# Kernel tuning notes

Hardware: AMD Instinct MI355X
Metric: run time of the kernel (lower is better)

## Reference

```python
import jax, jax.numpy as jnp
import numpy as np

BETA = 0.9


def setup_inputs() -> dict:
    key = jax.random.key(0)
    ks = jax.random.split(key, 9)
    B, T, D, H, C = 512, 2048, 64, 48, 3
    s = lambda k, shape, fan_in: jax.random.normal(k, shape, jnp.float32) / np.sqrt(fan_in)
    return {
        "x": jax.random.normal(ks[0], (B, T, D), jnp.float32),
        "W_enc": s(ks[1], (H, D), D),
        "b_enc": jnp.zeros((H,), jnp.float32),
        "W_mem": s(ks[2], (H, H), H),
        "b_mem": jnp.zeros((H,), jnp.float32),
        "W_dec": s(ks[3], (D, H), H),
        "b_dec": jnp.zeros((D,), jnp.float32),
        "W_cls": s(ks[4], (C, H), H),
        "b_cls": jnp.zeros((C,), jnp.float32),
    }


def _forward(x, W_enc, b_enc, W_mem, b_mem, W_dec, b_dec, W_cls, b_cls):
    B, T, D = x.shape
    H = W_enc.shape[0]
    # Precompute input drive for all steps in one big matmul: [B, T, H]
    u = jnp.einsum("btd,hd->bth", x, W_enc) + b_enc
    u_t = jnp.swapaxes(u, 0, 1)  # [T, B, H]

    def step(mem, u_step):
        cur = u_step + mem @ W_mem.T + b_mem
        mem = BETA * mem + (1.0 - BETA) * cur
        return mem, jax.nn.sigmoid(mem)

    mem0 = jnp.zeros((B, H), x.dtype)
    _, spikes = jax.lax.scan(step, mem0, u_t)  # spikes: [T, B, H]
    z = jnp.swapaxes(spikes, 0, 1)  # [B, T, H]
    recon = jnp.einsum("bth,dh->btd", z, W_dec) + b_dec
    logits = z.mean(axis=1) @ W_cls.T + b_cls
    return recon, logits, z


def reference(x, W_enc, b_enc, W_mem, b_mem, W_dec, b_dec, W_cls, b_cls):
    return _forward(x, W_enc, b_enc, W_mem, b_mem, W_dec, b_dec, W_cls, b_cls)
```

## Files before the change

### kernel.cpp

```cpp
#include <hip/hip_runtime.h>
#include <cstdint>
#include <cstddef>

#define B_ 512
#define T_ 2048
#define D_ 64
#define H_ 48
#define C_ 3
#define LCH 16
#define KCH 128
#define NC  65536
#define CPB 128
#define SMS 162

#define RECON_FLOATS ((size_t)B_ * T_ * D_)
#define LOGIT_FLOATS ((size_t)B_ * C_)
#define Z_OFF        (RECON_FLOATS + LOGIT_FLOATS)
#define A16_OFF  ((size_t)59768832)

__global__ __launch_bounds__(128) void k_enc(
    const float* __restrict__ x, const float* __restrict__ Wenc,
    const float* __restrict__ benc, const float* __restrict__ bmem,
    float* __restrict__ out)
{
    __shared__ float sx[128][68];
    __shared__ float sw[48][68];
    __shared__ float sbe[48];

    const int tid = threadIdx.x;

    {
        const float4* wf4 = reinterpret_cast<const float4*>(Wenc);
        #pragma unroll
        for (int m = 0; m < 6; ++m) {
            const int idx = tid + 128 * m;
            const int c = idx >> 4, d4 = idx & 15;
            *reinterpret_cast<float4*>(&sw[c][d4 * 4]) = wf4[idx];
        }
    }
    if (tid < 48) sbe[tid] = benc[tid] + bmem[tid];

    {
        const float4* xf4 = reinterpret_cast<const float4*>(x) + (size_t)blockIdx.x * 2048;
        #pragma unroll
        for (int m = 0; m < 16; ++m) {
            const int idx = tid + 128 * m;
            const int row = idx >> 4, d4 = idx & 15;
            *reinterpret_cast<float4*>(&sx[row][d4 * 4]) = xf4[idx];
        }
    }
    __syncthreads();

    const int lane = tid & 63;
    const int wv   = tid >> 6;
    const int rg   = lane >> 2;
    const int cg   = lane & 3;
    const int rowb = wv * 64 + rg;
    const int colb = cg * 12;

    float acc[4][12];
    {
        float bia[12];
        #pragma unroll
        for (int m = 0; m < 3; ++m)
            *reinterpret_cast<float4*>(&bia[4 * m]) = *reinterpret_cast<const float4*>(&sbe[colb + 4 * m]);
        #pragma unroll
        for (int k = 0; k < 4; ++k)
            #pragma unroll
            for (int i = 0; i < 12; ++i) acc[k][i] = bia[i];
    }

    #pragma unroll 2
    for (int d4 = 0; d4 < 16; ++d4) {
        float4 xf[4];
        #pragma unroll
        for (int k = 0; k < 4; ++k)
            xf[k] = *reinterpret_cast<const float4*>(&sx[rowb + 16 * k][d4 * 4]);
        #pragma unroll
        for (int i = 0; i < 12; ++i) {
            const float4 wvv = *reinterpret_cast<const float4*>(&sw[colb + i][d4 * 4]);
            #pragma unroll
            for (int k = 0; k < 4; ++k)
                acc[k][i] = fmaf(xf[k].x, wvv.x, fmaf(xf[k].y, wvv.y,
                             fmaf(xf[k].z, wvv.z, fmaf(xf[k].w, wvv.w, acc[k][i]))));
        }
    }

    const size_t row0 = (size_t)blockIdx.x * 128 + rowb;
    #pragma unroll
    for (int k = 0; k < 4; ++k) {
        float* dst = out + (row0 + 16 * k) * 48 + colb;
        #pragma unroll
        for (int m = 0; m < 3; ++m)
            *reinterpret_cast<float4*>(dst + 4 * m) =
                make_float4(acc[k][4 * m], acc[k][4 * m + 1], acc[k][4 * m + 2], acc[k][4 * m + 3]);
    }
}

__global__ __launch_bounds__(576) void k_powA(
    const float* __restrict__ Wmem, float* __restrict__ out)
{
    __shared__ float a0[48 * 49];
    __shared__ float a1[48 * 49];
    const int tid = threadIdx.x;

    for (int idx = tid; idx < 2304; idx += 576) {
        const int i = idx / 48, j = idx - i * 48;
        a0[i * 49 + j] = 0.1f * Wmem[idx] + (i == j ? 0.9f : 0.0f);
    }
    __syncthreads();

    float* src = a0;
    float* dst = a1;
    #pragma unroll 1
    for (int it = 0; it < 4; ++it) {
        float v[4];
        #pragma unroll
        for (int q = 0; q < 4; ++q) {
            const int o = tid + 576 * q;
            const int i = o / 48, j = o - i * 48;
            float acc = 0.f;
            #pragma unroll
            for (int k = 0; k < 48; ++k)
                acc = fmaf(src[i * 49 + k], src[k * 49 + j], acc);
            v[q] = acc;
        }
        #pragma unroll
        for (int q = 0; q < 4; ++q) {
            const int o = tid + 576 * q;
            const int i = o / 48, j = o - i * 48;
            dst[i * 49 + j] = v[q];
        }
        __syncthreads();
        float* t = src; src = dst; dst = t;
    }
    for (int idx = tid; idx < 2304; idx += 576) {
        const int i = idx / 48, j = idx - i * 48;
        out[A16_OFF + idx] = src[i * 49 + j];
    }
}

#define LOAD_UREG(sidx)                                                         \
    {                                                                           \
        const float* pb = u + (c0 + cbase) * 768 + (size_t)(sidx) * 48 + r0;    \
        _Pragma("unroll")                                                       \
        for (int j = 0; j < 8; ++j) {                                           \
            ureg[j][0] = pb[j * 768 + 0];                                       \
            ureg[j][1] = pb[j * 768 + 1];                                       \
            ureg[j][2] = pb[j * 768 + 2];                                       \
        }                                                                       \
    }

#define GEMM_STEP                                                               \
    float acc[3][8];                                                            \
    _Pragma("unroll")                                                           \
    for (int r = 0; r < 3; ++r)                                                 \
        _Pragma("unroll")                                                       \
        for (int j = 0; j < 8; ++j) acc[r][j] = ureg[j][r];                     \
    LOAD_UREG(s + 1 < LCH ? s + 1 : LCH - 1)                                    \
    _Pragma("unroll")                                                           \
    for (int k4 = 0; k4 < 12; ++k4) {                                           \
        float4 av[3];                                                           \
        _Pragma("unroll")                                                       \
        for (int r = 0; r < 3; ++r)                                             \
            av[r] = *reinterpret_cast<const float4*>(&sA[(r0 + r) * 52 + k4 * 4]); \
        float4 mv0[4], mv1[4];                                                  \
        _Pragma("unroll")                                                       \
        for (int kk = 0; kk < 4; ++kk) {                                        \
            mv0[kk] = *reinterpret_cast<const float4*>(&sM[(k4 * 4 + kk) * SMS + pcb]);     \
            mv1[kk] = *reinterpret_cast<const float4*>(&sM[(k4 * 4 + kk) * SMS + pcb + 4]); \
        }                                                                       \
        _Pragma("unroll")                                                       \
        for (int kk = 0; kk < 4; ++kk) {                                        \
            _Pragma("unroll")                                                   \
            for (int r = 0; r < 3; ++r) {                                       \
                const float a = kk == 0 ? av[r].x : kk == 1 ? av[r].y           \
                              : kk == 2 ? av[r].z : av[r].w;                    \
                acc[r][0] = fmaf(a, mv0[kk].x, acc[r][0]);                      \
                acc[r][1] = fmaf(a, mv0[kk].y, acc[r][1]);                      \
                acc[r][2] = fmaf(a, mv0[kk].z, acc[r][2]);                      \
                acc[r][3] = fmaf(a, mv0[kk].w, acc[r][3]);                      \
                acc[r][4] = fmaf(a, mv1[kk].x, acc[r][4]);                      \
                acc[r][5] = fmaf(a, mv1[kk].y, acc[r][5]);                      \
                acc[r][6] = fmaf(a, mv1[kk].z, acc[r][6]);                      \
                acc[r][7] = fmaf(a, mv1[kk].w, acc[r][7]);                      \
            }                                                                   \
        }                                                                       \
    }

#define WRITE_M                                                                 \
    __syncthreads();                                                            \
    _Pragma("unroll")                                                           \
    for (int r = 0; r < 3; ++r) {                                               \
        *reinterpret_cast<float4*>(&sM[(r0 + r) * SMS + pcb]) =                 \
            make_float4(acc[r][0], acc[r][1], acc[r][2], acc[r][3]);            \
        *reinterpret_cast<float4*>(&sM[(r0 + r) * SMS + pcb + 4]) =             \
            make_float4(acc[r][4], acc[r][5], acc[r][6], acc[r][7]);            \
    }                                                                           \
    __syncthreads();

__global__ __launch_bounds__(256) void k_scan(
    const float* __restrict__ Wmem, const float* __restrict__ A16g,
    const float* __restrict__ Wcls, const float* __restrict__ bcls,
    const float* __restrict__ u, float* __restrict__ z, float* __restrict__ logits)
{
    __shared__ float sA[48 * 52];
    __shared__ float sB[48 * 52];
    __shared__ float sM[48 * SMS];
    __shared__ float szs[48];

    const int tid = threadIdx.x;
    const int b   = blockIdx.x;

    for (int idx = tid; idx < 2304; idx += 256) {
        const int i = idx / 48, j = idx - i * 48;
        sA[i * 52 + j] = 0.1f * Wmem[idx] + (i == j ? 0.9f : 0.0f);
        sB[i * 52 + j] = A16g[idx];
    }
    for (int idx = tid; idx < 48 * SMS; idx += 256) sM[idx] = 0.f;

    const int rowg  = tid >> 4;
    const int colg  = tid & 15;
    const int r0    = rowg * 3;
    const int cbase = colg * 8;
    const int pcb   = colg * 10;
    const size_t c0 = (size_t)b * CPB;

    float ureg[8][3];
    LOAD_UREG(0)
    __syncthreads();

    #pragma unroll 1
    for (int s = 0; s < LCH; ++s) {
        GEMM_STEP
        WRITE_M
    }

    if (tid < 64) {
        const int h = tid < 48 ? tid : 0;
        float w16[48];
        #pragma unroll
        for (int j4 = 0; j4 < 12; ++j4) {
            const float4 w = *reinterpret_cast<const float4*>(&sB[h * 52 + 4 * j4]);
            w16[4 * j4 + 0] = w.x; w16[4 * j4 + 1] = w.y;
            w16[4 * j4 + 2] = w.z; w16[4 * j4 + 3] = w.w;
        }
        float E = 0.f;
        #pragma unroll 1
        for (int k = 0; k < KCH; ++k) {
            const int pck = (k >> 3) * 10 + (k & 7);
            const float s0v = (tid < 48) ? sM[h * SMS + pck] : 0.f;
            if (tid < 48) sM[h * SMS + pck] = E;
            float a0 = s0v, a1 = 0.f, a2 = 0.f, a3 = 0.f, a4 = 0.f, a5 = 0.f, a6 = 0.f, a7 = 0.f;
            #pragma unroll
            for (int g = 0; g < 6; ++g) {
                const int j = 8 * g;
                const float m0 = __int_as_float(__builtin_amdgcn_readlane(__float_as_int(E), j + 0));
                const float m1 = __int_as_float(__builtin_amdgcn_readlane(__float_as_int(E), j + 1));
                const float m2 = __int_as_float(__builtin_amdgcn_readlane(__float_as_int(E), j + 2));
                const float m3 = __int_as_float(__builtin_amdgcn_readlane(__float_as_int(E), j + 3));
                const float m4 = __int_as_float(__builtin_amdgcn_readlane(__float_as_int(E), j + 4));
                const float m5 = __int_as_float(__builtin_amdgcn_readlane(__float_as_int(E), j + 5));
                const float m6 = __int_as_float(__builtin_amdgcn_readlane(__float_as_int(E), j + 6));
                const float m7 = __int_as_float(__builtin_amdgcn_readlane(__float_as_int(E), j + 7));
                a0 = fmaf(m0, w16[j + 0], a0);
                a1 = fmaf(m1, w16[j + 1], a1);
                a2 = fmaf(m2, w16[j + 2], a2);
                a3 = fmaf(m3, w16[j + 3], a3);
                a4 = fmaf(m4, w16[j + 4], a4);
                a5 = fmaf(m5, w16[j + 5], a5);
                a6 = fmaf(m6, w16[j + 6], a6);
                a7 = fmaf(m7, w16[j + 7], a7);
            }
            E = ((a0 + a1) + (a2 + a3)) + ((a4 + a5) + (a6 + a7));
        }
    }
    __syncthreads();

    LOAD_UREG(0)
    float zrow[3];
    #pragma unroll
    for (int r = 0; r < 3; ++r) zrow[r] = 0.f;
    const float kExp = -0.14426950408889634f;

    #pragma unroll 1
    for (int s = 0; s < LCH; ++s) {
        GEMM_STEP
        {
            float* zb = z + (c0 + cbase) * 768 + (size_t)s * 48 + r0;
            #pragma unroll
            for (int j = 0; j < 8; ++j) {
                #pragma unroll
                for (int r = 0; r < 3; ++r) {
                    const float zq = __builtin_amdgcn_rcpf(1.0f + __builtin_amdgcn_exp2f(acc[r][j] * kExp));
                    zrow[r] += zq;
                    zb[j * 768 + r] = zq;
                }
            }
        }
        if (s + 1 < LCH) { WRITE_M }
    }
    __syncthreads();

    #pragma unroll
    for (int r = 0; r < 3; ++r)
        sM[(r0 + r) * SMS + colg] = zrow[r];
    __syncthreads();
    if (tid < 48) {
        float a = 0.f;
        #pragma unroll
        for (int c = 0; c < 16; ++c) a += sM[tid * SMS + c];
        szs[tid] = a;
    }
    __syncthreads();
    if (tid < C_) {
        float acc2 = 0.f;
        #pragma unroll
        for (int hh = 0; hh < 48; ++hh) acc2 = fmaf(szs[hh], Wcls[tid * 48 + hh], acc2);
        logits[(size_t)b * C_ + tid] = acc2 * (1.0f / (float)T_) + bcls[tid];
    }
}

__global__ __launch_bounds__(256) void k_dec(
    const float* __restrict__ Wdec, const float* __restrict__ bdec,
    float* __restrict__ out)
{
    __shared__ float sz[256][52];
    __shared__ float swT[48][68];
    __shared__ float sbd[64];

    const int tid = threadIdx.x;

    #pragma unroll
    for (int m = 0; m < 12; ++m) {
        const int idx = tid + 256 * m;
        const int d = idx / 48, hh = idx - d * 48;
        swT[hh][d] = Wdec[idx];
    }
    if (tid < 64) sbd[tid] = bdec[tid];

    {
        const float4* zf4 = reinterpret_cast<const float4*>(out + Z_OFF) + (size_t)blockIdx.x * 3072;
        #pragma unroll
        for (int m = 0; m < 12; ++m) {
            const int idx = tid + 256 * m;
            const int row = idx / 12, c4 = idx - row * 12;
            *reinterpret_cast<float4*>(&sz[row][c4 * 4]) = zf4[idx];
        }
    }
    __syncthreads();

    const int lane = tid & 63;
    const int wv   = tid >> 6;
    const int rg   = lane >> 3;
    const int cg   = lane & 7;
    const int rowb = wv * 64 + rg;
    const int colb = cg * 8;

    float acc[8][8];
    {
        float bd[8];
        *reinterpret_cast<float4*>(&bd[0]) = *reinterpret_cast<const float4*>(&sbd[colb]);
        *reinterpret_cast<float4*>(&bd[4]) = *reinterpret_cast<const float4*>(&sbd[colb + 4]);
        #pragma unroll
        for (int k = 0; k < 8; ++k)
            #pragma unroll
            for (int c = 0; c < 8; ++c) acc[k][c] = bd[c];
    }

    #pragma unroll 2
    for (int h4 = 0; h4 < 12; ++h4) {
        float4 zf[8];
        #pragma unroll
        for (int k = 0; k < 8; ++k)
            zf[k] = *reinterpret_cast<const float4*>(&sz[rowb + 8 * k][h4 * 4]);
        #pragma unroll
        for (int j = 0; j < 4; ++j) {
            const float4 w0 = *reinterpret_cast<const float4*>(&swT[h4 * 4 + j][colb]);
            const float4 w1 = *reinterpret_cast<const float4*>(&swT[h4 * 4 + j][colb + 4]);
            #pragma unroll
            for (int k = 0; k < 8; ++k) {
                const float zv = j == 0 ? zf[k].x : (j == 1 ? zf[k].y : (j == 2 ? zf[k].z : zf[k].w));
                acc[k][0] = fmaf(zv, w0.x, acc[k][0]);
                acc[k][1] = fmaf(zv, w0.y, acc[k][1]);
                acc[k][2] = fmaf(zv, w0.z, acc[k][2]);
                acc[k][3] = fmaf(zv, w0.w, acc[k][3]);
                acc[k][4] = fmaf(zv, w1.x, acc[k][4]);
                acc[k][5] = fmaf(zv, w1.y, acc[k][5]);
                acc[k][6] = fmaf(zv, w1.z, acc[k][6]);
                acc[k][7] = fmaf(zv, w1.w, acc[k][7]);
            }
        }
    }

    const size_t row0 = (size_t)blockIdx.x * 256 + rowb;
    #pragma unroll
    for (int k = 0; k < 8; ++k) {
        float* dst = out + (row0 + 8 * k) * 64 + colb;
        *reinterpret_cast<float4*>(dst)     = make_float4(acc[k][0], acc[k][1], acc[k][2], acc[k][3]);
        *reinterpret_cast<float4*>(dst + 4) = make_float4(acc[k][4], acc[k][5], acc[k][6], acc[k][7]);
    }
}

extern "C" void kernel_launch(void* const* d_in, const int* in_sizes, int n_in,
                              void* d_out, int out_size, void* d_ws, size_t ws_size,
                              hipStream_t stream) {
    const float* x    = (const float*)d_in[0];
    const float* Wenc = (const float*)d_in[1];
    const float* benc = (const float*)d_in[2];
    const float* Wmem = (const float*)d_in[3];
    const float* bmem = (const float*)d_in[4];
    const float* Wdec = (const float*)d_in[5];
    const float* bdec = (const float*)d_in[6];
    const float* Wcls = (const float*)d_in[7];
    const float* bcls = (const float*)d_in[8];
    float* out = (float*)d_out;

    k_powA<<<dim3(1), dim3(576), 0, stream>>>(Wmem, out);
    k_enc<<<dim3((B_ * T_) / 128), dim3(128), 0, stream>>>(x, Wenc, benc, bmem, out);
    k_scan<<<dim3(B_), dim3(256), 0, stream>>>(Wmem, out + A16_OFF, Wcls, bcls,
                                               out, out + Z_OFF, out + RECON_FLOATS);
    k_dec<<<dim3((B_ * T_) / 256), dim3(256), 0, stream>>>(Wdec, bdec, out);
}
```

Measured before the change: 480.8 us.

## Fuse A^16 power and decoder GEMM into scan kernel, reuse z buffer for u

Drops the single-block k_powA kernel and instead has every scan block compute A^16 redundantly in shared memory. It also fuses the decoder GEMM into the end of the scan kernel, reading z back per tile. The encoder now writes u directly into the z output region, which the scan overwrites in place. This removes two launches and a separate decoder pass, at the cost of redundant per-block matrix powers and a serialized decoder tail inside each scan block.

Measured after the change: 1.055 ms. +119.4%, slower.

```diff
diff --git a/kernel.cpp b/kernel.cpp
--- a/kernel.cpp
+++ b/kernel.cpp
@@ -9,19 +9,17 @@
 #define C_ 3
 #define LCH 16
 #define KCH 128
-#define NC  65536
 #define CPB 128
 #define SMS 162
 
 #define RECON_FLOATS ((size_t)B_ * T_ * D_)
 #define LOGIT_FLOATS ((size_t)B_ * C_)
 #define Z_OFF        (RECON_FLOATS + LOGIT_FLOATS)
-#define A16_OFF  ((size_t)59768832)
 
 __global__ __launch_bounds__(128) void k_enc(
     const float* __restrict__ x, const float* __restrict__ Wenc,
     const float* __restrict__ benc, const float* __restrict__ bmem,
-    float* __restrict__ out)
+    float* __restrict__ uout)
 {
     __shared__ float sx[128][68];
     __shared__ float sw[48][68];
@@ -89,54 +87,11 @@
     const size_t row0 = (size_t)blockIdx.x * 128 + rowb;
     #pragma unroll
     for (int k = 0; k < 4; ++k) {
-        float* dst = out + (row0 + 16 * k) * 48 + colb;
+        float* dst = uout + (row0 + 16 * k) * 48 + colb;
         #pragma unroll
         for (int m = 0; m < 3; ++m)
             *reinterpret_cast<float4*>(dst + 4 * m) =
                 make_float4(acc[k][4 * m], acc[k][4 * m + 1], acc[k][4 * m + 2], acc[k][4 * m + 3]);
-    }
-}
-
-__global__ __launch_bounds__(576) void k_powA(
-    const float* __restrict__ Wmem, float* __restrict__ out)
-{
-    __shared__ float a0[48 * 49];
-    __shared__ float a1[48 * 49];
-    const int tid = threadIdx.x;
-
-    for (int idx = tid; idx < 2304; idx += 576) {
-        const int i = idx / 48, j = idx - i * 48;
-        a0[i * 49 + j] = 0.1f * Wmem[idx] + (i == j ? 0.9f : 0.0f);
-    }
-    __syncthreads();
-
-    float* src = a0;
-    float* dst = a1;
-    #pragma unroll 1
-    for (int it = 0; it < 4; ++it) {
-        float v[4];
-        #pragma unroll
-        for (int q = 0; q < 4; ++q) {
-            const int o = tid + 576 * q;
-            const int i = o / 48, j = o - i * 48;
-            float acc = 0.f;
-            #pragma unroll
-            for (int k = 0; k < 48; ++k)
-                acc = fmaf(src[i * 49 + k], src[k * 49 + j], acc);
-            v[q] = acc;
-        }
-        #pragma unroll
-        for (int q = 0; q < 4; ++q) {
-            const int o = tid + 576 * q;
-            const int i = o / 48, j = o - i * 48;
-            dst[i * 49 + j] = v[q];
-        }
-        __syncthreads();
-        float* t = src; src = dst; dst = t;
-    }
-    for (int idx = tid; idx < 2304; idx += 576) {
-        const int i = idx / 48, j = idx - i * 48;
-        out[A16_OFF + idx] = src[i * 49 + j];
     }
 }
 
@@ -200,23 +155,62 @@
     __syncthreads();
 
 __global__ __launch_bounds__(256) void k_scan(
-    const float* __restrict__ Wmem, const float* __restrict__ A16g,
+    const float* __restrict__ Wmem,
     const float* __restrict__ Wcls, const float* __restrict__ bcls,
-    const float* __restrict__ u, float* __restrict__ z, float* __restrict__ logits)
+    const float* __restrict__ Wdec, const float* __restrict__ bdec,
+    float* __restrict__ zu,
+    float* __restrict__ recon,
+    float* __restrict__ logits)
 {
-    __shared__ float sA[48 * 52];
-    __shared__ float sB[48 * 52];
-    __shared__ float sM[48 * SMS];
+    __shared__ float smem[12768];
     __shared__ float szs[48];
+    float* sA = smem;
+    float* sB = smem + 2496;
+    float* sM = smem + 4992;
+    const float* u = zu;
 
     const int tid = threadIdx.x;
     const int b   = blockIdx.x;
 
     for (int idx = tid; idx < 2304; idx += 256) {
         const int i = idx / 48, j = idx - i * 48;
-        sA[i * 52 + j] = 0.1f * Wmem[idx] + (i == j ? 0.9f : 0.0f);
-        sB[i * 52 + j] = A16g[idx];
-    }
+        const float a = 0.1f * Wmem[idx] + (i == j ? 0.9f : 0.0f);
+        sA[i * 52 + j] = a;
+        sB[i * 52 + j] = a;
+    }
+    __syncthreads();
+    {
+        float* src = sB;
+        float* dst = sM;
+        #pragma unroll 1
+        for (int it = 0; it < 4; ++it) {
+            float v[9];
+            #pragma unroll
+            for (int q = 0; q < 9; ++q) {
+                const int o = tid + 256 * q;
+                const int i = o / 48, j = o - i * 48;
+                float a0 = 0.f, a1 = 0.f, a2 = 0.f, a3 = 0.f;
+                #pragma unroll 4
+                for (int k = 0; k < 48; k += 4) {
+                    a0 = fmaf(src[i * 52 + k + 0], src[(k + 0) * 52 + j], a0);
+                    a1 = fmaf(src[i * 52 + k + 1], src[(k + 1) * 52 + j], a1);
+                    a2 = fmaf(src[i * 52 + k + 2], src[(k + 2) * 52 + j], a2);
+                    a3 = fmaf(src[i * 52 + k + 3], src[(k + 3) * 52 + j], a3);
+                }
+                v[q] = (a0 + a1) + (a2 + a3);
+            }
+            __syncthreads();
+            #pragma unroll
+            for (int q = 0; q < 9; ++q) {
+                const int o = tid + 256 * q;
+                const int i = o / 48, j = o - i * 48;
+                dst[i * 52 + j] = v[q];
+            }
+            __syncthreads();
+            float* t = src; src = dst; dst = t;
+        }
+    }
+
     for (int idx = tid; idx < 48 * SMS; idx += 256) sM[idx] = 0.f;
 
     const int rowg  = tid >> 4;
@@ -287,7 +281,7 @@
     for (int s = 0; s < LCH; ++s) {
         GEMM_STEP
         {
-            float* zb = z + (c0 + cbase) * 768 + (size_t)s * 48 + r0;
+            float* zb = zu + (c0 + cbase) * 768 + (size_t)s * 48 + r0;
             #pragma unroll
             for (int j = 0; j < 8; ++j) {
                 #pragma unroll
@@ -301,6 +295,8 @@
         if (s + 1 < LCH) { WRITE_M }
     }
     __syncthreads();
+    __threadfence();
+    __syncthreads();
 
     #pragma unroll
     for (int r = 0; r < 3; ++r)
@@ -319,86 +315,78 @@
         for (int hh = 0; hh < 48; ++hh) acc2 = fmaf(szs[hh], Wcls[tid * 48 + hh], acc2);
         logits[(size_t)b * C_ + tid] = acc2 * (1.0f / (float)T_) + bcls[tid];
     }
-}
-
-__global__ __launch_bounds__(256) void k_dec(
-    const float* __restrict__ Wdec, const float* __restrict__ bdec,
-    float* __restrict__ out)
-{
-    __shared__ float sz[256][52];
-    __shared__ float swT[48][68];
-    __shared__ float sbd[64];
-
-    const int tid = threadIdx.x;
-
-    #pragma unroll
-    for (int m = 0; m < 12; ++m) {
-        const int idx = tid + 256 * m;
-        const int d = idx / 48, hh = idx - d * 48;
-        swT[hh][d] = Wdec[idx];
-    }
-    if (tid < 64) sbd[tid] = bdec[tid];
 
     {
-        const float4* zf4 = reinterpret_cast<const float4*>(out + Z_OFF) + (size_t)blockIdx.x * 3072;
-        #pragma unroll
-        for (int m = 0; m < 12; ++m) {
-            const int idx = tid + 256 * m;
-            const int row = idx / 12, c4 = idx - row * 12;
-            *reinterpret_cast<float4*>(&sz[row][c4 * 4]) = zf4[idx];
-        }
-    }
-    __syncthreads();
-
-    const int lane = tid & 63;
-    const int wv   = tid >> 6;
-    const int rg   = lane >> 3;
-    const int cg   = lane & 7;
-    const int rowb = wv * 64 + rg;
-    const int colb = cg * 8;
-
-    float acc[8][8];
-    {
-        float bd[8];
-        *reinterpret_cast<float4*>(&bd[0]) = *reinterpret_cast<const float4*>(&sbd[colb]);
-        *reinterpret_cast<float4*>(&bd[4]) = *reinterpret_cast<const float4*>(&sbd[colb + 4]);
-        #pragma unroll
-        for (int k = 0; k < 8; ++k)
-            #pragma unroll
-            for (int c = 0; c < 8; ++c) acc[k][c] = bd[c];
-    }
-
-    #pragma unroll 2
-    for (int h4 = 0; h4 < 12; ++h4) {
-        float4 zf[8];
-        #pragma unroll
-        for (int k = 0; k < 8; ++k)
-            zf[k] = *reinterpret_cast<const float4*>(&sz[rowb + 8 * k][h4 * 4]);
-        #pragma unroll
-        for (int j = 0; j < 4; ++j) {
-            const float4 w0 = *reinterpret_cast<const float4*>(&swT[h4 * 4 + j][colb]);
-            const float4 w1 = *reinterpret_cast<const float4*>(&swT[h4 * 4 + j][colb + 4]);
-            #pragma unroll
-            for (int k = 0; k < 8; ++k) {
-                const float zv = j == 0 ? zf[k].x : (j == 1 ? zf[k].y : (j == 2 ? zf[k].z : zf[k].w));
-                acc[k][0] = fmaf(zv, w0.x, acc[k][0]);
-                acc[k][1] = fmaf(zv, w0.y, acc[k][1]);
-                acc[k][2] = fmaf(zv, w0.z, acc[k][2]);
-                acc[k][3] = fmaf(zv, w0.w, acc[k][3]);
-                acc[k][4] = fmaf(zv, w1.x, acc[k][4]);
-                acc[k][5] = fmaf(zv, w1.y, acc[k][5]);
-                acc[k][6] = fmaf(zv, w1.z, acc[k][6]);
-                acc[k][7] = fmaf(zv, w1.w, acc[k][7]);
-            }
-        }
-    }
-
-    const size_t row0 = (size_t)blockIdx.x * 256 + rowb;
-    #pragma unroll
-    for (int k = 0; k < 8; ++k) {
-        float* dst = out + (row0 + 8 * k) * 64 + colb;
-        *reinterpret_cast<float4*>(dst)     = make_float4(acc[k][0], acc[k][1], acc[k][2], acc[k][3]);
-        *reinterpret_cast<float4*>(dst + 4) = make_float4(acc[k][4], acc[k][5], acc[k][6], acc[k][7]);
+        float* swT = smem;
+        float* sbd = smem + 3072;
+        float* szt = smem + 3200;
+
+        for (int idx = tid; idx < 3072; idx += 256) {
+            const int d = idx / 48, hh = idx - d * 48;
+            swT[hh * 64 + d] = Wdec[idx];
+        }
+        if (tid < 64) sbd[tid] = bdec[tid];
+
+        const int lane = tid & 63;
+        const int wv4  = tid >> 6;
+        const int rg   = lane >> 3;
+        const int cg   = lane & 7;
+        const int rowb = wv4 * 32 + rg;
+        const int colb = cg * 8;
+        const float* zsrc = zu + c0 * 768;
+        float* rb = recon + (size_t)b * T_ * 64;
+
+        #pragma unroll 1
+        for (int tile = 0; tile < 16; ++tile) {
+            __syncthreads();
+            const float4* zf4 = reinterpret_cast<const float4*>(zsrc + (size_t)tile * 6144);
+            #pragma unroll
+            for (int m = 0; m < 6; ++m) {
+                const int idx4 = tid + 256 * m;
+                const int rloc = idx4 / 12, c4 = idx4 - rloc * 12;
+                *reinterpret_cast<float4*>(&szt[rloc * 52 + c4 * 4]) = zf4[idx4];
+            }
+            __syncthreads();
+
+            float acc2[4][8];
+            #pragma unroll
+            for (int k = 0; k < 4; ++k) {
+                #pragma unroll
+                for (int c = 0; c < 8; ++c) acc2[k][c] = sbd[colb + c];
+            }
+
+            #pragma unroll 2
+            for (int h4 = 0; h4 < 12; ++h4) {
+                float4 zf[4];
+                #pragma unroll
+                for (int k = 0; k < 4; ++k)
+                    zf[k] = *reinterpret_cast<const float4*>(&szt[(rowb + 8 * k) * 52 + h4 * 4]);
+                #pragma unroll
+                for (int j = 0; j < 4; ++j) {
+                    const float4 w0 = *reinterpret_cast<const float4*>(&swT[(h4 * 4 + j) * 64 + colb]);
+                    const float4 w1 = *reinterpret_cast<const float4*>(&swT[(h4 * 4 + j) * 64 + colb + 4]);
+                    #pragma unroll
+                    for (int k = 0; k < 4; ++k) {
+                        const float zv = j == 0 ? zf[k].x : (j == 1 ? zf[k].y : (j == 2 ? zf[k].z : zf[k].w));
+                        acc2[k][0] = fmaf(zv, w0.x, acc2[k][0]);
+                        acc2[k][1] = fmaf(zv, w0.y, acc2[k][1]);
+                        acc2[k][2] = fmaf(zv, w0.z, acc2[k][2]);
+                        acc2[k][3] = fmaf(zv, w0.w, acc2[k][3]);
+                        acc2[k][4] = fmaf(zv, w1.x, acc2[k][4]);
+                        acc2[k][5] = fmaf(zv, w1.y, acc2[k][5]);
+                        acc2[k][6] = fmaf(zv, w1.z, acc2[k][6]);
+                        acc2[k][7] = fmaf(zv, w1.w, acc2[k][7]);
+                    }
+                }
+            }
+
+            #pragma unroll
+            for (int k = 0; k < 4; ++k) {
+                float* dst = rb + (size_t)(tile * 128 + rowb + 8 * k) * 64 + colb;
+                *reinterpret_cast<float4*>(dst)     = make_float4(acc2[k][0], acc2[k][1], acc2[k][2], acc2[k][3]);
+                *reinterpret_cast<float4*>(dst + 4) = make_float4(acc2[k][4], acc2[k][5], acc2[k][6], acc2[k][7]);
+            }
+        }
     }
 }
 
@@ -416,9 +404,7 @@
     const float* bcls = (const float*)d_in[8];
     float* out = (float*)d_out;
 
-    k_powA<<<dim3(1), dim3(576), 0, stream>>>(Wmem, out);
-    k_enc<<<dim3((B_ * T_) / 128), dim3(128), 0, stream>>>(x, Wenc, benc, bmem, out);
-    k_scan<<<dim3(B_), dim3(256), 0, stream>>>(Wmem, out + A16_OFF, Wcls, bcls,
-                                               out, out + Z_OFF, out + RECON_FLOATS);
-    k_dec<<<dim3((B_ * T_) / 256), dim3(256), 0, stream>>>(Wdec, bdec, out);
+    k_enc<<<dim3((B_ * T_) / 128), dim3(128), 0, stream>>>(x, Wenc, benc, bmem, out + Z_OFF);
+    k_scan<<<dim3(B_), dim3(256), 0, stream>>>(Wmem, Wcls, bcls, Wdec, bdec,
+                                               out + Z_OFF, out, out + RECON_FLOATS);
 }
```
